# Kernel tuning notes

Measured on AMD Instinct MI355X. Metric: run time of the kernel, lower is better.

Reference implementation:

```python
import jax, jax.numpy as jnp
import numpy as np

EMBED = 256
NHEAD = 8
DFF = 1024
NLAYERS = 1
B, H, W, WS = 4, 128, 128, 16


def _layernorm(x, g, b, eps=1e-5):
    mu = jnp.mean(x, axis=-1, keepdims=True)
    var = jnp.var(x, axis=-1, keepdims=True)
    return (x - mu) * jax.lax.rsqrt(var + eps) * g + b


def _mha(q, k, v, in_w, in_b, out_w, out_b, kpm=None):
    # torch nn.MultiheadAttention (batch_first) with dropout=0
    Bn, L, C = q.shape
    dh = C // NHEAD
    wq, wk, wv = jnp.split(in_w, 3, axis=0)
    bq, bk, bv = jnp.split(in_b, 3, axis=0)
    qh = (q @ wq.T + bq).reshape(Bn, L, NHEAD, dh)
    kh = (k @ wk.T + bk).reshape(Bn, k.shape[1], NHEAD, dh)
    vh = (v @ wv.T + bv).reshape(Bn, v.shape[1], NHEAD, dh)
    scores = jnp.einsum('bqhd,bkhd->bhqk', qh, kh) * (dh ** -0.5)
    if kpm is not None:  # True == masked key
        scores = jnp.where(kpm[:, None, None, :], -jnp.inf, scores)
    attn = jax.nn.softmax(scores, axis=-1)
    out = jnp.einsum('bhqk,bkhd->bqhd', attn, vh).reshape(Bn, L, C)
    return out @ out_w.T + out_b


def _enc_layer(q, k, v, p, kpm=None):
    # post-norm AxisPermutedEncoderLayer, dropout=0
    (in_w, in_b, out_w, out_b, l1w, l1b, l2w, l2b, g1, b1, g2, b2) = p
    src = v + _mha(q, k, v, in_w, in_b, out_w, out_b, kpm)
    src = _layernorm(src, g1, b1)
    ff = jax.nn.relu(src @ l1w.T + l1b) @ l2w.T + l2b
    return _layernorm(src + ff, g2, b2)


def _forward(backbone_memory, defe_feature_filtered, window_size, glob_pos_embed,
             rel_w1, rel_b1, rel_w2, rel_b2,
             in_proj_w, in_proj_b, out_proj_w, out_proj_b,
             lin1_w, lin1_b, lin2_w, lin2_b, ln1_g, ln1_b, ln2_g, ln2_b):
    Bb, C, Hh, Ww = backbone_memory.shape
    ws = window_size
    nwh, nww = Hh // ws, Ww // ws
    nw, T = nwh * nww, ws * ws
    p = (in_proj_w, in_proj_b, out_proj_w, out_proj_b,
         lin1_w, lin1_b, lin2_w, lin2_b, ln1_g, ln1_b, ln2_g, ln2_b)
    # relative position embedding: MLP over normalized in-window (y,x) coords
    ys, xs = jnp.meshgrid(jnp.arange(ws), jnp.arange(ws), indexing='ij')
    coords = jnp.stack([ys, xs], -1).reshape(T, 2).astype(backbone_memory.dtype) / max(ws - 1, 1)
    rel = jax.nn.relu(coords @ rel_w1.T + rel_b1) @ rel_w2.T + rel_b2  # [T,C]
    # window partition -> [B, nw, T, C]
    feats = backbone_memory.reshape(Bb, C, nwh, ws, nww, ws).transpose(0, 2, 4, 1, 3, 5)
    feats = feats.reshape(Bb, nw, C, T).transpose(0, 1, 3, 2)
    gp = glob_pos_embed.reshape(C, nwh, ws, nww, ws).transpose(1, 3, 0, 2, 4)
    gp = gp.reshape(nw, C, T).transpose(0, 2, 1)[None]  # [1,nw,T,C]
    pos = jnp.broadcast_to(gp + rel[None, None], (Bb, nw, T, C))
    # window validity via max-pool of binary map
    pooled = defe_feature_filtered.reshape(Bb, 1, nwh, ws, nww, ws).max(axis=(3, 5))
    valid = pooled.reshape(Bb, nw) > 0  # bool [B,nw]
    x = feats
    for _ in range(NLAYERS):
        # within-window attention over T tokens
        wi = x.reshape(Bb * nw, T, C)
        wp = pos.reshape(Bb * nw, T, C)
        x = _enc_layer(wi + wp, wi + wp, wi, p).reshape(Bb, nw, T, C)
        # cross-window attention over nw windows (per token position)
        ci = x.transpose(0, 2, 1, 3).reshape(Bb * T, nw, C)
        cp = pos.transpose(0, 2, 1, 3).reshape(Bb * T, nw, C)
        kpm = jnp.broadcast_to(~valid[:, None, :], (Bb, T, nw)).reshape(Bb * T, nw)
        x = _enc_layer(ci + cp, ci + cp, ci, p, kpm).reshape(Bb, T, nw, C).transpose(0, 2, 1, 3)
    enc = x.transpose(0, 1, 3, 2).reshape(Bb, nw, C, ws, ws)
    enc = enc * valid.astype(x.dtype)[:, :, None, None, None]
    upd = enc.reshape(Bb, nwh, nww, C, ws, ws).transpose(0, 3, 1, 4, 2, 5).reshape(Bb, C, Hh, Ww)
    return backbone_memory + upd, valid


def setup_inputs() -> dict:
    key = jax.random.key(0)
    ks = jax.random.split(key, 16)
    C, s = EMBED, 0.02
    inp = {}
    inp['backbone_memory'] = jax.random.normal(ks[0], (B, C, H, W), jnp.float32)
    inp['defe_feature_filtered'] = (jax.random.uniform(ks[1], (B, 1, H, W)) < 0.002).astype(jnp.float32)
    inp['window_size'] = WS
    inp['glob_pos_embed'] = jax.random.normal(ks[2], (C, H, W), jnp.float32) * s
    inp['rel_w1'] = jax.random.normal(ks[3], (64, 2), jnp.float32) * s
    inp['rel_b1'] = jnp.zeros((64,), jnp.float32)
    inp['rel_w2'] = jax.random.normal(ks[4], (C, 64), jnp.float32) * s
    inp['rel_b2'] = jnp.zeros((C,), jnp.float32)
    inp['in_proj_w'] = jax.random.normal(ks[5], (3 * C, C), jnp.float32) * s
    inp['in_proj_b'] = jnp.zeros((3 * C,), jnp.float32)
    inp['out_proj_w'] = jax.random.normal(ks[6], (C, C), jnp.float32) * s
    inp['out_proj_b'] = jnp.zeros((C,), jnp.float32)
    inp['lin1_w'] = jax.random.normal(ks[7], (DFF, C), jnp.float32) * s
    inp['lin1_b'] = jnp.zeros((DFF,), jnp.float32)
    inp['lin2_w'] = jax.random.normal(ks[8], (C, DFF), jnp.float32) * s
    inp['lin2_b'] = jnp.zeros((C,), jnp.float32)
    inp['ln1_g'] = jnp.ones((C,), jnp.float32)
    inp['ln1_b'] = jnp.zeros((C,), jnp.float32)
    inp['ln2_g'] = jnp.ones((C,), jnp.float32)
    inp['ln2_b'] = jnp.zeros((C,), jnp.float32)
    return inp


def reference(backbone_memory, defe_feature_filtered, window_size, glob_pos_embed,
              rel_w1, rel_b1, rel_w2, rel_b2,
              in_proj_w, in_proj_b, out_proj_w, out_proj_b,
              lin1_w, lin1_b, lin2_w, lin2_b, ln1_g, ln1_b, ln2_g, ln2_b):
    return _forward(backbone_memory, defe_feature_filtered, window_size, glob_pos_embed,
                    rel_w1, rel_b1, rel_w2, rel_b2,
                    in_proj_w, in_proj_b, out_proj_w, out_proj_b,
                    lin1_w, lin1_b, lin2_w, lin2_b, ln1_g, ln1_b, ln2_g, ln2_b)
```

## Files before the change

kernel.cpp:

```cpp
#include <hip/hip_runtime.h>
#include <hip/hip_bf16.h>

#define CEMB 256
#define NHEAD 8
#define DHEAD 32
#define DFF 1024
#define BB 4
#define HH 128
#define WW 128
#define WSZ 16
#define NWH 8
#define NW 64
#define TT 256
#define NTOK (BB*NW*TT)

typedef __attribute__((ext_vector_type(8))) short bf16x8;
typedef __attribute__((ext_vector_type(4))) float f32x4;

__device__ __forceinline__ float bf2f(unsigned short u){
    union { float f; unsigned int i; } v; v.i = ((unsigned int)u) << 16; return v.f;
}
__device__ __forceinline__ unsigned short f2bf(float f){
    union { float f; unsigned int i; } v; v.f = f;
    unsigned int r = v.i + 0x7fffu + ((v.i >> 16) & 1u);
    return (unsigned short)(r >> 16);
}
__device__ __forceinline__ unsigned int cvtpk_bf16(float lo, float hi){
    unsigned int r;
    asm("v_cvt_pk_bf16_f32 %0, %1, %2" : "=v"(r) : "v"(lo), "v"(hi));
    return r;
}
__device__ __forceinline__ void unpack8(uint4 v, float* f){
    f[0]=bf2f((unsigned short)(v.x & 0xffff)); f[1]=bf2f((unsigned short)(v.x>>16));
    f[2]=bf2f((unsigned short)(v.y & 0xffff)); f[3]=bf2f((unsigned short)(v.y>>16));
    f[4]=bf2f((unsigned short)(v.z & 0xffff)); f[5]=bf2f((unsigned short)(v.z>>16));
    f[6]=bf2f((unsigned short)(v.w & 0xffff)); f[7]=bf2f((unsigned short)(v.w>>16));
}
__device__ __forceinline__ void async_copy16(const void* g, void* l){
    __builtin_amdgcn_global_load_lds(
        (const __attribute__((address_space(1))) unsigned int*)g,
        (__attribute__((address_space(3))) unsigned int*)l, 16, 0, 0);
}
__device__ __forceinline__ int sgran(int c, int g){ return c*32 + (g ^ (c & 31)); }

__global__ __launch_bounds__(256) void rel_kernel(const float* __restrict__ rw1,
    const float* __restrict__ rb1, const float* __restrict__ rw2,
    const float* __restrict__ rb2, float* __restrict__ rel)
{
    __shared__ float hsh[64];
    int t = blockIdx.x, c = threadIdx.x;
    int ty = t >> 4, tx = t & 15;
    if (c < 64){
        float y = ty*(1.0f/15.0f), xx = tx*(1.0f/15.0f);
        hsh[c] = fmaxf(y*rw1[2*c] + xx*rw1[2*c+1] + rb1[c], 0.0f);
    }
    __syncthreads();
    float acc = rb2[c];
    #pragma unroll 16
    for (int k = 0; k < 64; ++k) acc += hsh[k]*rw2[c*64 + k];
    rel[t*256 + c] = acc;
}

__global__ __launch_bounds__(256) void posT_kernel(const float* __restrict__ gp,
    const float* __restrict__ rel, unsigned short* __restrict__ pos)
{
    __shared__ float tile[8192];
    const int w  = blockIdx.x >> 3;
    const int cq = (blockIdx.x >> 1) & 3, th = blockIdx.x & 1;
    const int c0 = cq << 6, t0 = th << 7, y0 = th << 3;
    const int wh = w >> 3, wwi = w & 7;
    const int tid = threadIdx.x;
    const float* gpb = gp + (size_t)c0*(HH*WW) + (size_t)(wh*16 + y0)*WW + wwi*16;
    #pragma unroll
    for (int i = 0; i < 8; ++i){
        int n = i*256 + tid, slot = n & 31, c = n >> 5;
        int yl = slot >> 2, xg = slot & 3;
        float4 v = *(const float4*)(gpb + (size_t)c*(HH*WW) + yl*WW + xg*4);
        *(float4*)&tile[sgran(c, slot)*4] = v;
    }
    __syncthreads();
    #pragma unroll
    for (int i = 0; i < 4; ++i){
        int n = i*256 + tid, j = n & 7, tl = n >> 3;
        int g = tl >> 2, e = tl & 3;
        const float* rl = rel + (t0 + tl)*256 + c0 + j*8;
        unsigned short o[8];
        #pragma unroll
        for (int m = 0; m < 8; ++m)
            o[m] = f2bf(tile[sgran(j*8 + m, g)*4 + e] + rl[m]);
        *(uint4*)&pos[((size_t)w*256 + t0 + tl)*CEMB + c0 + j*8] = *(uint4*)o;
    }
}

__global__ __launch_bounds__(256) void valid_kernel(const float* __restrict__ defe,
    float* __restrict__ validf, float* __restrict__ tail)
{
    __shared__ float red[4];
    int bw = blockIdx.x; int b = bw >> 6, w = bw & 63;
    int t = threadIdx.x; int ty = t >> 4, tx = t & 15;
    int wh = w >> 3, wwi = w & 7;
    float v = defe[(size_t)b*(HH*WW) + (wh*16+ty)*WW + wwi*16 + tx];
    int lane = t & 63, wave = t >> 6;
    for (int off = 1; off < 64; off <<= 1) v = fmaxf(v, __shfl_xor(v, off));
    if (lane == 0) red[wave] = v;
    __syncthreads();
    if (t == 0){
        float m = fmaxf(fmaxf(red[0], red[1]), fmaxf(red[2], red[3]));
        float r = (m > 0.0f) ? 1.0f : 0.0f;
        validf[bw] = r;
        tail[bw] = r;
    }
}

__global__ __launch_bounds__(256) void partition_kernel(const float* __restrict__ bb,
    unsigned short* __restrict__ x)
{
    __shared__ float tile[8192];
    const int bw = blockIdx.x >> 3;
    const int b = bw >> 6, w = bw & 63;
    const int cq = (blockIdx.x >> 1) & 3, th = blockIdx.x & 1;
    const int c0 = cq << 6, t0 = th << 7, y0 = th << 3;
    const int wh = w >> 3, wwi = w & 7;
    const int tid = threadIdx.x;
    const float* bbb = bb + ((size_t)(b*CEMB + c0))*(HH*WW) + (size_t)(wh*16 + y0)*WW + wwi*16;
    #pragma unroll
    for (int i = 0; i < 8; ++i){
        int n = i*256 + tid, slot = n & 31, c = n >> 5;
        int yl = slot >> 2, xg = slot & 3;
        float4 v = *(const float4*)(bbb + (size_t)c*(HH*WW) + yl*WW + xg*4);
        *(float4*)&tile[sgran(c, slot)*4] = v;
    }
    __syncthreads();
    #pragma unroll
    for (int i = 0; i < 4; ++i){
        int n = i*256 + tid, j = n & 7, tl = n >> 3;
        int g = tl >> 2, e = tl & 3;
        unsigned short o[8];
        #pragma unroll
        for (int m = 0; m < 8; ++m)
            o[m] = f2bf(tile[sgran(j*8 + m, g)*4 + e]);
        *(uint4*)&x[((size_t)bw*256 + t0 + tl)*CEMB + c0 + j*8] = *(uint4*)o;
    }
}

__global__ __launch_bounds__(256) void wcvt_kernel(const float* __restrict__ w,
    unsigned short* __restrict__ o, int n4)
{
    int i = blockIdx.x*256 + threadIdx.x;
    if (i < n4){
        float4 v = ((const float4*)w)[i];
        ushort4 u;
        u.x = f2bf(v.x); u.y = f2bf(v.y); u.z = f2bf(v.z); u.w = f2bf(v.w);
        ((ushort4*)o)[i] = u;
    }
}

__global__ __launch_bounds__(256) void addpos_kernel(const unsigned short* __restrict__ x,
    const unsigned short* __restrict__ pos, unsigned short* __restrict__ xp)
{
    size_t i = ((size_t)blockIdx.x*256 + threadIdx.x) * 8;
    size_t tok = i >> 8; int c = (int)(i & 255);
    size_t pi = ((tok & 16383) << 8) + c;
    uint4 xv = *(const uint4*)&x[i];
    uint4 pv = *(const uint4*)&pos[pi];
    float xf[8], pf[8]; unpack8(xv, xf); unpack8(pv, pf);
    unsigned short o[8];
    #pragma unroll
    for (int j = 0; j < 8; ++j) o[j] = f2bf(xf[j] + pf[j]);
    *(uint4*)&xp[i] = *(uint4*)o;
}

__global__ __launch_bounds__(256) void gemm_mfma(
    const unsigned short* __restrict__ A,
    const unsigned short* __restrict__ A2, int nsplit, int ldA,
    const unsigned short* __restrict__ W, int K,
    const float* __restrict__ bias,
    unsigned short* __restrict__ out, int ldO, int relu)
{
    __shared__ unsigned short As[128*32];
    __shared__ unsigned short Bs[128*32];
    const int m0 = blockIdx.x << 7, n0 = blockIdx.y << 7;
    const int tid = threadIdx.x;
    const int lane = tid & 63, wave = tid >> 6;
    const int wm = wave & 1, wn = wave >> 1;
    const int fl = lane & 15, quad = lane >> 4;

    const unsigned short* Ap = ((n0 < nsplit) ? A : A2) + (size_t)m0*ldA;
    const unsigned short* Wp = W + (size_t)n0*K;

    const int c0 = tid, c1 = tid + 256;
    const int r0 = c0 >> 2, o0 = ((c0 & 3) ^ ((c0 >> 3) & 3)) << 3;
    const int r1 = c1 >> 2, o1 = ((c1 & 3) ^ ((c1 >> 3) & 3)) << 3;
    const int sw = (quad ^ ((fl >> 1) & 3)) << 3;

    f32x4 acc[4][4] = {};

    for (int k0 = 0; k0 < K; k0 += 32){
        async_copy16(Ap + (size_t)r0*ldA + k0 + o0, &As[c0 << 3]);
        async_copy16(Ap + (size_t)r1*ldA + k0 + o1, &As[c1 << 3]);
        async_copy16(Wp + (size_t)r0*K   + k0 + o0, &Bs[c0 << 3]);
        async_copy16(Wp + (size_t)r1*K   + k0 + o1, &Bs[c1 << 3]);
        __syncthreads();
        bf16x8 av[4], bv[4];
        #pragma unroll
        for (int i = 0; i < 4; ++i){
            av[i] = *(const bf16x8*)&As[(wm*64 + i*16 + fl)*32 + sw];
            bv[i] = *(const bf16x8*)&Bs[(wn*64 + i*16 + fl)*32 + sw];
        }
        #pragma unroll
        for (int i = 0; i < 4; ++i)
            #pragma unroll
            for (int j = 0; j < 4; ++j)
                acc[i][j] = __builtin_amdgcn_mfma_f32_16x16x32_bf16(av[i], bv[j], acc[i][j], 0, 0, 0);
        __syncthreads();
    }

    float bj[4];
    #pragma unroll
    for (int j = 0; j < 4; ++j) bj[j] = bias[n0 + wn*64 + j*16 + fl];
    #pragma unroll
    for (int i = 0; i < 4; ++i){
        int mrow = m0 + wm*64 + i*16 + quad*4;
        #pragma unroll
        for (int j = 0; j < 4; ++j){
            int col = n0 + wn*64 + j*16 + fl;
            #pragma unroll
            for (int r = 0; r < 4; ++r){
                float v = acc[i][j][r] + bj[j];
                if (relu) v = fmaxf(v, 0.0f);
                out[(size_t)(mrow + r)*ldO + col] = f2bf(v);
            }
        }
    }
}

__global__ __launch_bounds__(256, 3) void gemm_ln(
    const unsigned short* __restrict__ A, int K,
    const unsigned short* __restrict__ W,
    const float* __restrict__ bias,
    const unsigned short* __restrict__ resid,
    const float* __restrict__ g, const float* __restrict__ b,
    unsigned short* __restrict__ out)
{
    __shared__ unsigned short As[64*32];
    __shared__ unsigned short Bs[256*32];
    __shared__ float psum[4][64];
    __shared__ float psq[4][64];
    const int m0 = blockIdx.x << 6;
    const int tid = threadIdx.x, lane = tid & 63, wave = tid >> 6;
    const int wn = wave;
    const int fl = lane & 15, quad = lane >> 4;

    const unsigned short* Ap = A + (size_t)m0*K;

    const int ra = tid >> 2, oa = ((tid & 3) ^ ((tid >> 3) & 3)) << 3;
    const int sw = (quad ^ ((fl >> 1) & 3)) << 3;

    f32x4 acc[4][4] = {};

    for (int k0 = 0; k0 < K; k0 += 32){
        async_copy16(Ap + (size_t)ra*K + k0 + oa, &As[tid << 3]);
        #pragma unroll
        for (int t = 0; t < 4; ++t){
            int c = tid + t*256;
            int r = c >> 2, o = ((c & 3) ^ ((c >> 3) & 3)) << 3;
            async_copy16(W + (size_t)r*K + k0 + o, &Bs[c << 3]);
        }
        __syncthreads();
        bf16x8 av[4], bv[4];
        #pragma unroll
        for (int i = 0; i < 4; ++i)
            av[i] = *(const bf16x8*)&As[(i*16 + fl)*32 + sw];
        #pragma unroll
        for (int j = 0; j < 4; ++j)
            bv[j] = *(const bf16x8*)&Bs[(wn*64 + j*16 + fl)*32 + sw];
        #pragma unroll
        for (int i = 0; i < 4; ++i)
            #pragma unroll
            for (int j = 0; j < 4; ++j)
                acc[i][j] = __builtin_amdgcn_mfma_f32_16x16x32_bf16(av[i], bv[j], acc[i][j], 0, 0, 0);
        __syncthreads();
    }

    float bcol[4], gcol[4], bbcol[4];
    #pragma unroll
    for (int j = 0; j < 4; ++j){
        int col = wn*64 + j*16 + fl;
        bcol[j] = bias[col]; gcol[j] = g[col]; bbcol[j] = b[col];
    }
    float s[4][4] = {{0}}, sq[4][4] = {{0}};
    #pragma unroll
    for (int i = 0; i < 4; ++i)
        #pragma unroll
        for (int r = 0; r < 4; ++r){
            int row = m0 + i*16 + quad*4 + r;
            #pragma unroll
            for (int j = 0; j < 4; ++j){
                float h = acc[i][j][r] + bcol[j]
                        + bf2f(resid[(size_t)row*256 + wn*64 + j*16 + fl]);
                acc[i][j][r] = h;
                s[i][r] += h; sq[i][r] += h*h;
            }
        }
    #pragma unroll
    for (int i = 0; i < 4; ++i)
        #pragma unroll
        for (int r = 0; r < 4; ++r){
            float ss = s[i][r], qq = sq[i][r];
            ss += __shfl_xor(ss, 1); qq += __shfl_xor(qq, 1);
            ss += __shfl_xor(ss, 2); qq += __shfl_xor(qq, 2);
            ss += __shfl_xor(ss, 4); qq += __shfl_xor(qq, 4);
            ss += __shfl_xor(ss, 8); qq += __shfl_xor(qq, 8);
            if (fl == 0){
                int lr = i*16 + quad*4 + r;
                psum[wn][lr] = ss; psq[wn][lr] = qq;
            }
        }
    __syncthreads();
    #pragma unroll
    for (int i = 0; i < 4; ++i)
        #pragma unroll
        for (int r = 0; r < 4; ++r){
            int lr = i*16 + quad*4 + r;
            float mu  = (psum[0][lr] + psum[1][lr] + psum[2][lr] + psum[3][lr]) * (1.0f/256.0f);
            float var = (psq[0][lr] + psq[1][lr] + psq[2][lr] + psq[3][lr]) * (1.0f/256.0f) - mu*mu;
            float rstd = rsqrtf(var + 1e-5f);
            #pragma unroll
            for (int j = 0; j < 4; ++j){
                int col = wn*64 + j*16 + fl;
                out[(size_t)(m0 + lr)*256 + col] =
                    f2bf((acc[i][j][r] - mu)*rstd*gcol[j] + bbcol[j]);
            }
        }
}

template<int L, bool CROSS>
__global__ __launch_bounds__(256, 3) void attn_mfma(const unsigned short* __restrict__ qkv,
    unsigned short* __restrict__ attn_out, const float* __restrict__ validf)
{
    constexpr int QW  = (L == 256) ? 64 : 16;
    constexpr int MI  = QW / 16;
    constexpr int VTS = L + 8;
    constexpr int LOG = (L == 256) ? 8 : 6;
    __shared__ unsigned short Ks[L*32];
    __shared__ unsigned short Vt[32*VTS];

    const int s = blockIdx.x, h = blockIdx.y;
    int base, stride;
    if (CROSS){ base = (s >> 8)*16384 + (s & 255); stride = 256; }
    else      { base = s << 8; stride = 1; }
    const int tid = threadIdx.x, lane = tid & 63, wave = tid >> 6;
    const int fl = lane & 15, quad = lane >> 4;
    const float scale = 0.17677669529663687f;

    for (int cid = tid; cid < L*4; cid += 256){
        int j = cid >> 2, part = (cid & 3) ^ ((cid >> 3) & 3);
        async_copy16(qkv + (size_t)(base + j*stride)*768 + 256 + h*32 + part*8, &Ks[cid*8]);
    }
    for (int e = tid; e < L*4; e += 256){
        int j = e & (L-1), dp = e >> LOG;
        uint4 vv = *(const uint4*)(qkv + (size_t)(base + j*stride)*768 + 512 + h*32 + dp*8);
        unsigned short tmp[8]; *(uint4*)tmp = vv;
        #pragma unroll
        for (int d = 0; d < 8; ++d) Vt[(dp*8 + d)*VTS + j] = tmp[d];
    }
    __syncthreads();

    bf16x8 qf[MI];
    #pragma unroll
    for (int mi = 0; mi < MI; ++mi){
        int q = wave*QW + mi*16 + fl;
        qf[mi] = *(const bf16x8*)(qkv + (size_t)(base + q*stride)*768 + h*32 + quad*8);
    }
    float vm[4][4];
    if (CROSS){
        #pragma unroll
        for (int nj = 0; nj < 4; ++nj){
            float4 v4 = *(const float4*)&validf[(s >> 8)*64 + nj*16 + quad*4];
            vm[nj][0] = v4.x; vm[nj][1] = v4.y; vm[nj][2] = v4.z; vm[nj][3] = v4.w;
        }
    }

    f32x4 oacc[MI][2] = {};
    float lpart[MI] = {};
    const int sw = (quad ^ ((fl >> 1) & 3)) << 3;
    const int la = fl | ((quad & 1) << 5);
    const int lb = la + 16;

    for (int j0 = 0; j0 < L; j0 += 64){
        bf16x8 kf[4];
        #pragma unroll
        for (int nj = 0; nj < 4; ++nj)
            kf[nj] = *(const bf16x8*)&Ks[(j0 + nj*16 + fl)*32 + sw];
        unsigned int pk[MI][4][2];
        #pragma unroll
        for (int mi = 0; mi < MI; ++mi){
            f32x4 sacc[4] = {};
            #pragma unroll
            for (int nj = 0; nj < 4; ++nj)
                sacc[nj] = __builtin_amdgcn_mfma_f32_16x16x32_bf16(kf[nj], qf[mi], sacc[nj], 0, 0, 0);
            #pragma unroll
            for (int nj = 0; nj < 4; ++nj){
                float p[4];
                #pragma unroll
                for (int r = 0; r < 4; ++r){
                    float pv = __expf(sacc[nj][r] * scale);
                    if (CROSS) pv *= vm[nj][r];
                    p[r] = pv;
                    lpart[mi] += pv;
                }
                pk[mi][nj][0] = cvtpk_bf16(p[0], p[1]);
                pk[mi][nj][1] = cvtpk_bf16(p[2], p[3]);
            }
        }
        #pragma unroll
        for (int kk = 0; kk < 2; ++kk){
            bf16x8 vf[2];
            #pragma unroll
            for (int nd = 0; nd < 2; ++nd)
                vf[nd] = *(const bf16x8*)&Vt[(nd*16 + fl)*VTS + j0 + kk*32 + quad*8];
            #pragma unroll
            for (int mi = 0; mi < MI; ++mi){
                unsigned int a0 = __shfl(pk[mi][2*kk  ][0], la, 64);
                unsigned int a1 = __shfl(pk[mi][2*kk  ][1], la, 64);
                unsigned int a2 = __shfl(pk[mi][2*kk  ][0], lb, 64);
                unsigned int a3 = __shfl(pk[mi][2*kk  ][1], lb, 64);
                unsigned int b0 = __shfl(pk[mi][2*kk+1][0], la, 64);
                unsigned int b1 = __shfl(pk[mi][2*kk+1][1], la, 64);
                unsigned int b2 = __shfl(pk[mi][2*kk+1][0], lb, 64);
                unsigned int b3 = __shfl(pk[mi][2*kk+1][1], lb, 64);
                const bool lo = quad < 2;
                union { unsigned int u[4]; bf16x8 v; } pu;
                pu.u[0] = lo ? a0 : b0;
                pu.u[1] = lo ? a1 : b1;
                pu.u[2] = lo ? a2 : b2;
                pu.u[3] = lo ? a3 : b3;
                #pragma unroll
                for (int nd = 0; nd < 2; ++nd)
                    oacc[mi][nd] = __builtin_amdgcn_mfma_f32_16x16x32_bf16(pu.v, vf[nd], oacc[mi][nd], 0, 0, 0);
            }
        }
    }

    #pragma unroll
    for (int mi = 0; mi < MI; ++mi){
        float l = lpart[mi];
        l += __shfl_xor(l, 16);
        l += __shfl_xor(l, 32);
        l = 1.0f / l;
        float li[4];
        #pragma unroll
        for (int r = 0; r < 4; ++r)
            li[r] = __shfl(l, quad*4 + r, 64);
        #pragma unroll
        for (int nd = 0; nd < 2; ++nd)
            #pragma unroll
            for (int r = 0; r < 4; ++r){
                int q = wave*QW + mi*16 + quad*4 + r;
                attn_out[(size_t)(base + q*stride)*CEMB + h*32 + nd*16 + fl] =
                    f2bf(oacc[mi][nd][r] * li[r]);
            }
    }
}

__global__ __launch_bounds__(256) void scatter_kernel(const float* __restrict__ bb,
    const unsigned short* __restrict__ x, const float* __restrict__ validf,
    float* __restrict__ out)
{
    __shared__ float tile[8192];
    const int bw = blockIdx.x >> 3;
    const int b = bw >> 6, w = bw & 63;
    const int cq = (blockIdx.x >> 1) & 3, th = blockIdx.x & 1;
    const int c0 = cq << 6, t0 = th << 7, y0 = th << 3;
    const int wh = w >> 3, wwi = w & 7;
    const int tid = threadIdx.x;
    const float vf = validf[bw];
    #pragma unroll
    for (int i = 0; i < 4; ++i){
        int n = i*256 + tid, j = n & 7, tl = n >> 3;
        int g = tl >> 2, e = tl & 3;
        uint4 xv = *(const uint4*)&x[((size_t)bw*256 + t0 + tl)*CEMB + c0 + j*8];
        float f[8]; unpack8(xv, f);
        #pragma unroll
        for (int m = 0; m < 8; ++m)
            tile[sgran(j*8 + m, g)*4 + e] = f[m];
    }
    __syncthreads();
    const size_t gbase = ((size_t)(b*CEMB + c0))*(HH*WW) + (size_t)(wh*16 + y0)*WW + wwi*16;
    #pragma unroll
    for (int i = 0; i < 8; ++i){
        int n = i*256 + tid, slot = n & 31, c = n >> 5;
        int yl = slot >> 2, xg = slot & 3;
        size_t gi = gbase + (size_t)c*(HH*WW) + yl*WW + xg*4;
        float4 bv = *(const float4*)(bb + gi);
        float4 xv = *(const float4*)&tile[sgran(c, slot)*4];
        float4 ov;
        ov.x = bv.x + vf*xv.x; ov.y = bv.y + vf*xv.y;
        ov.z = bv.z + vf*xv.z; ov.w = bv.w + vf*xv.w;
        *(float4*)(out + gi) = ov;
    }
}

extern "C" void kernel_launch(void* const* d_in, const int* in_sizes, int n_in,
                              void* d_out, int out_size, void* d_ws, size_t ws_size,
                              hipStream_t stream)
{
    (void)in_sizes; (void)n_in; (void)out_size; (void)ws_size;
    const float* backbone = (const float*)d_in[0];
    const float* defe     = (const float*)d_in[1];
    const float* gpe      = (const float*)d_in[3];
    const float* rw1 = (const float*)d_in[4];
    const float* rb1 = (const float*)d_in[5];
    const float* rw2 = (const float*)d_in[6];
    const float* rb2 = (const float*)d_in[7];
    const float* ipw = (const float*)d_in[8];
    const float* ipb = (const float*)d_in[9];
    const float* opw = (const float*)d_in[10];
    const float* opb = (const float*)d_in[11];
    const float* l1w = (const float*)d_in[12];
    const float* l1b = (const float*)d_in[13];
    const float* l2w = (const float*)d_in[14];
    const float* l2b = (const float*)d_in[15];
    const float* g1  = (const float*)d_in[16];
    const float* b1  = (const float*)d_in[17];
    const float* g2  = (const float*)d_in[18];
    const float* b2  = (const float*)d_in[19];

    char* ws = (char*)d_ws;
    unsigned short* pos    = (unsigned short*)(ws);
    unsigned short* x      = (unsigned short*)(ws +   8388608);
    unsigned short* qkv    = (unsigned short*)(ws +  41943040);
    unsigned short* shared_= (unsigned short*)(ws + 142606336);
    float*          validf = (float*)(ws + 176160768);
    unsigned short* ipw16  = (unsigned short*)(ws + 176161792);
    unsigned short* opw16  = (unsigned short*)(ws + 176555008);
    unsigned short* l1w16  = (unsigned short*)(ws + 176686080);
    unsigned short* l2w16  = (unsigned short*)(ws + 177210368);
    float*          rel    = (float*)(ws + 177734656);
    unsigned short* src = qkv;
    unsigned short* ff  = qkv + 16777216;
    float* outf = (float*)d_out;

    wcvt_kernel<<<192, 256, 0, stream>>>(ipw, ipw16, 49152);
    wcvt_kernel<<< 64, 256, 0, stream>>>(opw, opw16, 16384);
    wcvt_kernel<<<256, 256, 0, stream>>>(l1w, l1w16, 65536);
    wcvt_kernel<<<256, 256, 0, stream>>>(l2w, l2w16, 65536);
    rel_kernel<<<256, 256, 0, stream>>>(rw1, rb1, rw2, rb2, rel);
    posT_kernel<<<512, 256, 0, stream>>>(gpe, rel, pos);
    valid_kernel<<<BB*NW, 256, 0, stream>>>(defe, validf, outf + (size_t)BB*CEMB*HH*WW);
    partition_kernel<<<2048, 256, 0, stream>>>(backbone, x);

    for (int layer = 0; layer < 2; ++layer){
        addpos_kernel<<<8192, 256, 0, stream>>>(x, pos, shared_);
        gemm_mfma<<<dim3(512, 6), 256, 0, stream>>>(shared_, x, 512, CEMB, ipw16, CEMB, ipb, qkv, 768, 0);
        if (layer == 0)
            attn_mfma<256, false><<<dim3(BB*NW, NHEAD), 256, 0, stream>>>(qkv, shared_, validf);
        else
            attn_mfma<64, true><<<dim3(BB*TT, NHEAD), 256, 0, stream>>>(qkv, shared_, validf);
        gemm_ln<<<dim3(1024, 1), 256, 0, stream>>>(shared_, CEMB, opw16, opb, x, g1, b1, src);
        for (int ch = 0; ch < 2; ++ch){
            const int BIG = 1 << 30;
            unsigned short* srcC = src + (size_t)ch*8388608;
            gemm_mfma<<<dim3(256, 8), 256, 0, stream>>>(srcC, srcC, BIG, CEMB, l1w16, CEMB, l1b, ff, DFF, 1);
            gemm_ln<<<dim3(512, 1), 256, 0, stream>>>(ff, DFF, l2w16, l2b, srcC, g2, b2,
                                                      x + (size_t)ch*8388608);
        }
    }
    scatter_kernel<<<2048, 256, 0, stream>>>(backbone, x, validf, outf);
}
```

Before: 792.4 us.

## Fuse FFN linear1+ReLU+linear2+residual+LayerNorm into one kernel

Replaces the chunked two-kernel FFN (a GEMM writing the 1024-wide hidden activation to global memory, then a GEMM+LayerNorm reading it back) with one kernel per 64-token tile. The kernel computes the hidden activation in chunks of 64 columns, stages each chunk in LDS with an XOR swizzle, and accumulates the second GEMM in registers. The goal is to drop the global round trip of the large intermediate and the extra launches. In exchange, each block re-reads both weight matrices from cache, holds many registers (the src fragments plus the accumulators), and syncs twice per chunk, so occupancy may be lower.

Result: slower. 901.6 us (+13.8%).

```diff
diff --git a/kernel.cpp b/kernel.cpp
--- a/kernel.cpp
+++ b/kernel.cpp
@@ -328,6 +328,126 @@
             #pragma unroll
             for (int j = 0; j < 4; ++j){
                 int col = wn*64 + j*16 + fl;
+                out[(size_t)(m0 + lr)*256 + col] =
+                    f2bf((acc[i][j][r] - mu)*rstd*gcol[j] + bbcol[j]);
+            }
+        }
+}
+
+__global__ __launch_bounds__(256) void ffn_fused(
+    const unsigned short* __restrict__ src,
+    const unsigned short* __restrict__ w1,
+    const float* __restrict__ b1,
+    const unsigned short* __restrict__ w2,
+    const float* __restrict__ b2,
+    const float* __restrict__ g, const float* __restrict__ b,
+    unsigned short* __restrict__ out)
+{
+    __shared__ unsigned short hlds[64*64];
+    __shared__ float psum[4][64];
+    __shared__ float psq[4][64];
+    const int m0 = blockIdx.x << 6;
+    const int tid = threadIdx.x, lane = tid & 63, wave = tid >> 6;
+    const int fl = lane & 15, quad = lane >> 4;
+
+    bf16x8 qf[4][8];
+    #pragma unroll
+    for (int mi = 0; mi < 4; ++mi)
+        #pragma unroll
+        for (int kf = 0; kf < 8; ++kf)
+            qf[mi][kf] = *(const bf16x8*)&src[(size_t)(m0 + mi*16 + fl)*256 + kf*32 + quad*8];
+
+    f32x4 acc[4][4] = {};
+    const int gwr = wave*2 + (quad >> 1);
+    const int who = (quad & 1) << 2;
+
+    for (int c = 0; c < 16; ++c){
+        const int j0 = c << 6;
+        bf16x8 w1f[8];
+        #pragma unroll
+        for (int kf = 0; kf < 8; ++kf)
+            w1f[kf] = *(const bf16x8*)&w1[(size_t)(j0 + wave*16 + fl)*256 + kf*32 + quad*8];
+        float4 b1v = *(const float4*)&b1[j0 + wave*16 + quad*4];
+        #pragma unroll
+        for (int mi = 0; mi < 4; ++mi){
+            f32x4 sacc = {};
+            #pragma unroll
+            for (int kf = 0; kf < 8; ++kf)
+                sacc = __builtin_amdgcn_mfma_f32_16x16x32_bf16(w1f[kf], qf[mi][kf], sacc, 0, 0, 0);
+            float h0 = fmaxf(sacc[0] + b1v.x, 0.0f);
+            float h1 = fmaxf(sacc[1] + b1v.y, 0.0f);
+            float h2 = fmaxf(sacc[2] + b1v.z, 0.0f);
+            float h3 = fmaxf(sacc[3] + b1v.w, 0.0f);
+            int r_ = mi*16 + fl;
+            int gb = r_*64 + ((gwr ^ (fl & 7)) << 3) + who;
+            *(unsigned int*)&hlds[gb    ] = cvtpk_bf16(h0, h1);
+            *(unsigned int*)&hlds[gb + 2] = cvtpk_bf16(h2, h3);
+        }
+        __syncthreads();
+        #pragma unroll
+        for (int kk = 0; kk < 2; ++kk){
+            bf16x8 hf[4], w2f[4];
+            #pragma unroll
+            for (int mi = 0; mi < 4; ++mi)
+                hf[mi] = *(const bf16x8*)&hlds[(mi*16 + fl)*64 + (((kk*4 + quad) ^ (fl & 7)) << 3)];
+            #pragma unroll
+            for (int nd = 0; nd < 4; ++nd)
+                w2f[nd] = *(const bf16x8*)&w2[(size_t)(wave*64 + nd*16 + fl)*1024 + j0 + kk*32 + quad*8];
+            #pragma unroll
+            for (int mi = 0; mi < 4; ++mi)
+                #pragma unroll
+                for (int nd = 0; nd < 4; ++nd)
+                    acc[mi][nd] = __builtin_amdgcn_mfma_f32_16x16x32_bf16(hf[mi], w2f[nd], acc[mi][nd], 0, 0, 0);
+        }
+        __syncthreads();
+    }
+
+    float bcol[4], gcol[4], bbcol[4];
+    #pragma unroll
+    for (int j = 0; j < 4; ++j){
+        int col = wave*64 + j*16 + fl;
+        bcol[j] = b2[col]; gcol[j] = g[col]; bbcol[j] = b[col];
+    }
+    float s[4][4] = {{0}}, sq[4][4] = {{0}};
+    #pragma unroll
+    for (int i = 0; i < 4; ++i)
+        #pragma unroll
+        for (int r = 0; r < 4; ++r){
+            int row = m0 + i*16 + quad*4 + r;
+            #pragma unroll
+            for (int j = 0; j < 4; ++j){
+                float h = acc[i][j][r] + bcol[j]
+                        + bf2f(src[(size_t)row*256 + wave*64 + j*16 + fl]);
+                acc[i][j][r] = h;
+                s[i][r] += h; sq[i][r] += h*h;
+            }
+        }
+    #pragma unroll
+    for (int i = 0; i < 4; ++i)
+        #pragma unroll
+        for (int r = 0; r < 4; ++r){
+            float ss = s[i][r], qq = sq[i][r];
+            ss += __shfl_xor(ss, 1); qq += __shfl_xor(qq, 1);
+            ss += __shfl_xor(ss, 2); qq += __shfl_xor(qq, 2);
+            ss += __shfl_xor(ss, 4); qq += __shfl_xor(qq, 4);
+            ss += __shfl_xor(ss, 8); qq += __shfl_xor(qq, 8);
+            if (fl == 0){
+                int lr = i*16 + quad*4 + r;
+                psum[wave][lr] = ss; psq[wave][lr] = qq;
+            }
+        }
+    __syncthreads();
+    #pragma unroll
+    for (int i = 0; i < 4; ++i)
+        #pragma unroll
+        for (int r = 0; r < 4; ++r){
+            int lr = i*16 + quad*4 + r;
+            float mu  = (psum[0][lr] + psum[1][lr] + psum[2][lr] + psum[3][lr]) * (1.0f/256.0f);
+            float var = (psq[0][lr] + psq[1][lr] + psq[2][lr] + psq[3][lr]) * (1.0f/256.0f) - mu*mu;
+            float rstd = rsqrtf(var + 1e-5f);
+            #pragma unroll
+            for (int j = 0; j < 4; ++j){
+                int col = wave*64 + j*16 + fl;
                 out[(size_t)(m0 + lr)*256 + col] =
                     f2bf((acc[i][j][r] - mu)*rstd*gcol[j] + bbcol[j]);
             }
@@ -538,7 +658,6 @@
     unsigned short* l2w16  = (unsigned short*)(ws + 177210368);
     float*          rel    = (float*)(ws + 177734656);
     unsigned short* src = qkv;
-    unsigned short* ff  = qkv + 16777216;
     float* outf = (float*)d_out;
 
     wcvt_kernel<<<192, 256, 0, stream>>>(ipw, ipw16, 49152);
@@ -558,13 +677,7 @@
         else
             attn_mfma<64, true><<<dim3(BB*TT, NHEAD), 256, 0, stream>>>(qkv, shared_, validf);
         gemm_ln<<<dim3(1024, 1), 256, 0, stream>>>(shared_, CEMB, opw16, opb, x, g1, b1, src);
-        for (int ch = 0; ch < 2; ++ch){
-            const int BIG = 1 << 30;
-            unsigned short* srcC = src + (size_t)ch*8388608;
-            gemm_mfma<<<dim3(256, 8), 256, 0, stream>>>(srcC, srcC, BIG, CEMB, l1w16, CEMB, l1b, ff, DFF, 1);
-            gemm_ln<<<dim3(512, 1), 256, 0, stream>>>(ff, DFF, l2w16, l2b, srcC, g2, b2,
-                                                      x + (size_t)ch*8388608);
-        }
+        ffn_fused<<<1024, 256, 0, stream>>>(src, l1w16, l1b, l2w16, l2b, g2, b2, x);
     }
     scatter_kernel<<<2048, 256, 0, stream>>>(backbone, x, validf, outf);
 }
```
